# Kernel tuning notes

Measured on AMD Instinct MI355X. Metric: run time of the kernel, lower is better.

Reference implementation:

```python
import jax, jax.numpy as jnp
import numpy as np
from jax import lax

B, C, H, W = 4, 128, 64, 64
D = C // 2          # VSSBlock hidden_dim
DI = 2 * D          # SS2D d_inner (expand=2)
N = 16              # d_state
R = max(D // 16, 1) # dt_rank
K = 4               # scan directions

def dwconv(x, w, b):
    y = lax.conv_general_dilated(x, w, (1, 1), [(1, 1), (1, 1)],
        dimension_numbers=('NCHW', 'OIHW', 'NCHW'), feature_group_count=x.shape[1])
    return y + b[None, :, None, None]

def layer_norm(x, g, b, eps=1e-5):
    mu = jnp.mean(x, axis=-1, keepdims=True)
    var = jnp.var(x, axis=-1, keepdims=True)
    return (x - mu) * lax.rsqrt(var + eps) * g + b

def selective_scan(u, delta, A, Bs, Cs, Dp):
    # u, delta: (B,K,DI,L); Bs, Cs: (B,K,N,L); A: (K,DI,N); Dp: (K,DI)
    uT = jnp.moveaxis(u, -1, 0)
    dT = jnp.moveaxis(delta, -1, 0)
    BT = jnp.moveaxis(Bs, -1, 0)
    CT = jnp.moveaxis(Cs, -1, 0)
    h0 = jnp.zeros(u.shape[:3] + (A.shape[-1],), u.dtype)
    def step(h, inp):
        u_t, d_t, B_t, C_t = inp
        dA = jnp.exp(d_t[..., None] * A)                       # (B,K,DI,N)
        h = dA * h + (d_t * u_t)[..., None] * B_t[:, :, None, :]
        return h, jnp.einsum('bkdn,bkn->bkd', h, C_t)
    _, ys = lax.scan(step, h0, (uT, dT, BT, CT))
    return jnp.moveaxis(ys, 0, -1) + Dp[None, :, :, None] * u  # (B,K,DI,L)

def ss2d(x, in_proj_w, conv_w, conv_b, x_proj_w, dt_w, dt_b, A_logs, Ds, on_g, on_b, out_proj_w):
    # x: (B,H,W,D)
    b, h, w, _ = x.shape
    L = h * w
    xz = x @ in_proj_w.T                                       # (B,H,W,2*DI)
    xc, z = jnp.split(xz, 2, axis=-1)
    xc = jnp.transpose(xc, (0, 3, 1, 2))                       # (B,DI,H,W)
    xc = jax.nn.silu(dwconv(xc, conv_w, conv_b))
    x1 = xc.reshape(b, DI, L)                                  # row-major scan
    x2 = jnp.transpose(xc, (0, 1, 3, 2)).reshape(b, DI, L)     # col-major scan
    xs = jnp.stack([x1, x2, x1[:, :, ::-1], x2[:, :, ::-1]], axis=1)  # (B,K,DI,L)
    x_dbl = jnp.einsum('bkdl,kcd->bkcl', xs, x_proj_w)
    dts, Bsx, Csx = jnp.split(x_dbl, [R, R + N], axis=2)
    delta = jax.nn.softplus(jnp.einsum('bkrl,kdr->bkdl', dts, dt_w) + dt_b[None, :, :, None])
    A = -jnp.exp(A_logs).reshape(K, DI, N)
    out_y = selective_scan(xs, delta, A, Bsx, Csx, Ds.reshape(K, DI))  # (B,K,DI,L)
    inv_y = out_y[:, 2:4, :, ::-1]
    wh_y = jnp.transpose(out_y[:, 1].reshape(b, DI, w, h), (0, 1, 3, 2)).reshape(b, DI, L)
    invwh_y = jnp.transpose(inv_y[:, 1].reshape(b, DI, w, h), (0, 1, 3, 2)).reshape(b, DI, L)
    y = out_y[:, 0] + inv_y[:, 0] + wh_y + invwh_y             # (B,DI,L)
    y = jnp.transpose(y, (0, 2, 1)).reshape(b, h, w, DI)
    y = layer_norm(y, on_g, on_b) * jax.nn.silu(z)
    return y @ out_proj_w.T                                    # (B,H,W,D)

def _forward(x, dw_w, dw_b, scale, ln1_g, ln1_b, in_proj_w, conv_w, conv_b, x_proj_w, dt_w, dt_b, A_logs, Ds, out_norm_g, out_norm_b, out_proj_w, in_gamma, in_beta):
    xd = dwconv(x, dw_w, dw_b)
    x_1, x_2 = jnp.split(xd, 2, axis=1)
    def branch(xi):
        xp = jnp.transpose(xi, (0, 2, 3, 1))                   # (B,H,W,D)
        y = xp + ss2d(layer_norm(xp, ln1_g, ln1_b), in_proj_w, conv_w, conv_b,
                      x_proj_w, dt_w, dt_b, A_logs, Ds, out_norm_g, out_norm_b, out_proj_w)
        return scale * xi + jnp.transpose(y, (0, 3, 1, 2))
    xo = jnp.concatenate([branch(x_1), branch(x_2)], axis=1)
    mu = jnp.mean(xo, axis=(2, 3), keepdims=True)              # InstanceNorm2d(affine)
    var = jnp.var(xo, axis=(2, 3), keepdims=True)
    xo = (xo - mu) * lax.rsqrt(var + 1e-5) * in_gamma[None, :, None, None] + in_beta[None, :, None, None]
    return jnp.where(xo > 0, xo, 0.01 * xo)                    # LeakyReLU(0.01)

def setup_inputs():
    ks = jax.random.split(jax.random.key(0), 12)
    f = lambda k, shp, s=0.02: jax.random.normal(k, shp, jnp.float32) * s
    return dict(
        x=jax.random.normal(ks[0], (B, C, H, W), jnp.float32),
        dw_w=f(ks[1], (C, 1, 3, 3), 0.1), dw_b=f(ks[2], (C,), 0.1),
        scale=jnp.ones((1,), jnp.float32),
        ln1_g=jnp.ones((D,), jnp.float32), ln1_b=jnp.zeros((D,), jnp.float32),
        in_proj_w=f(ks[3], (2 * DI, D)),
        conv_w=f(ks[4], (DI, 1, 3, 3), 0.1), conv_b=f(ks[5], (DI,), 0.1),
        x_proj_w=f(ks[6], (K, R + 2 * N, DI)),
        dt_w=f(ks[7], (K, DI, R), 0.1), dt_b=f(ks[8], (K, DI), 0.1),
        A_logs=f(ks[9], (K * DI, N), 0.5), Ds=jnp.ones((K * DI,), jnp.float32),
        out_norm_g=jnp.ones((DI,), jnp.float32), out_norm_b=jnp.zeros((DI,), jnp.float32),
        out_proj_w=f(ks[10], (D, DI)),
        in_gamma=jnp.ones((C,), jnp.float32), in_beta=jnp.zeros((C,), jnp.float32),
    )

def reference(x, dw_w, dw_b, scale, ln1_g, ln1_b, in_proj_w, conv_w, conv_b, x_proj_w, dt_w, dt_b, A_logs, Ds, out_norm_g, out_norm_b, out_proj_w, in_gamma, in_beta):
    return _forward(x, dw_w, dw_b, scale, ln1_g, ln1_b, in_proj_w, conv_w, conv_b, x_proj_w, dt_w, dt_b, A_logs, Ds, out_norm_g, out_norm_b, out_proj_w, in_gamma, in_beta)
```

## Files before the change

kernel.cpp:

```cpp
#include <hip/hip_runtime.h>
#include <hip/hip_bf16.h>


__device__ __forceinline__ float LD(const void* p, size_t i, bool isb) {
  if (isb) {
    unsigned short u = ((const unsigned short*)p)[i];
    return __uint_as_float(((unsigned)u) << 16);
  }
  return ((const float*)p)[i];
}
__device__ __forceinline__ unsigned short f2bf(float f) {
  unsigned u = __float_as_uint(f);
  u = (u + 0x7FFFu + ((u >> 16) & 1u)) >> 16;
  return (unsigned short)u;
}
__device__ __forceinline__ float silu_(float x) { return x / (1.f + __expf(-x)); }
__device__ __forceinline__ float softplus_(float x) {
  return x > 20.f ? x : __logf(1.f + __expf(x));
}
#define EXP2R(x) __builtin_amdgcn_exp2f(x)

__global__ void kdet(const void* x, int* flag) {
  if (threadIdx.x == 0 && blockIdx.x == 0) {
    const unsigned short* xs = (const unsigned short*)x;
    int bad = 0;
    for (int i = 0; i < 64; ++i) {
      int e = (xs[2 * i] >> 7) & 0xFF;
      if (e > 150 || e < 100) bad++;
    }
    *flag = (bad >= 16) ? 0 : 1;
  }
}

__global__ __launch_bounds__(256) void k0_conv_ln(
    const void* x, const void* dww, const void* dwb, const void* lg, const void* lb,
    const int* __restrict__ flag,
    float* __restrict__ T1, float* __restrict__ T2)
{
  bool isb = (*flag != 0);
  int e = blockIdx.x >> 6, h = blockIdx.x & 63;
  int b = e & 3, br = e >> 2;
  int t = threadIdx.x;
  __shared__ float sIn[3][64][67];
  for (int idx = t; idx < 3 * 64; idx += 256) {
    int r = idx >> 6, d = idx & 63;
    sIn[r][d][0] = 0.f; sIn[r][d][65] = 0.f;
  }
  for (int idx = t; idx < 3 * 64 * 64; idx += 256) {
    int r = idx >> 12, rem = idx & 4095, d = rem >> 6, w = rem & 63;
    int hh = h + r - 1;
    float v = 0.f;
    if (hh >= 0 && hh < 64) v = LD(x, ((size_t)(b * 128 + br * 64 + d) * 64 + hh) * 64 + w, isb);
    sIn[r][d][1 + w] = v;
  }
  __syncthreads();
  int w = t >> 2, g = t & 3;
  float vals[16]; float psum = 0.f, psq = 0.f;
#pragma unroll
  for (int j = 0; j < 16; ++j) {
    int d = g * 16 + j, c = br * 64 + d;
    float s = LD(dwb, c, isb);
#pragma unroll
    for (int kh = 0; kh < 3; ++kh)
#pragma unroll
      for (int kw = 0; kw < 3; ++kw)
        s += LD(dww, c * 9 + kh * 3 + kw, isb) * sIn[kh][d][w + kw];
    vals[j] = s; psum += s; psq += s * s;
  }
  size_t base = ((size_t)e * 4096 + h * 64) * 64 + (size_t)t * 16;
#pragma unroll
  for (int j4 = 0; j4 < 4; ++j4) {
    float4 o; o.x = vals[j4*4]; o.y = vals[j4*4+1]; o.z = vals[j4*4+2]; o.w = vals[j4*4+3];
    *(float4*)(T1 + base + j4 * 4) = o;
  }
  __shared__ float sS[64][4], sQ[64][4];
  sS[w][g] = psum; sQ[w][g] = psq;
  __syncthreads();
  float m = (sS[w][0] + sS[w][1] + sS[w][2] + sS[w][3]) * (1.f / 64.f);
  float q = (sQ[w][0] + sQ[w][1] + sQ[w][2] + sQ[w][3]) * (1.f / 64.f);
  float rs = rsqrtf(q - m * m + 1e-5f);
#pragma unroll
  for (int j4 = 0; j4 < 4; ++j4) {
    float tmp[4];
#pragma unroll
    for (int jj = 0; jj < 4; ++jj) {
      int j = j4 * 4 + jj; int d = g * 16 + j;
      tmp[jj] = (vals[j] - m) * rs * LD(lg, d, isb) + LD(lb, d, isb);
    }
    float4 o; o.x = tmp[0]; o.y = tmp[1]; o.z = tmp[2]; o.w = tmp[3];
    *(float4*)(T2 + base + j4 * 4) = o;
  }
}

__global__ __launch_bounds__(256) void k2_inproj(
    const float* __restrict__ T2, const void* Wip, const int* __restrict__ flag,
    float* __restrict__ T3, float* __restrict__ T4)
{
  bool isb = (*flag != 0);
  int mt = blockIdx.x, ct = blockIdx.y;
  int t = threadIdx.x;
  __shared__ float sA[64][68];
  __shared__ float sB[64][68];
  int row0 = mt * 64;
  for (int q = t; q < 1024; q += 256) {
    int l = q >> 4, d4 = (q & 15) * 4;
    float4 v = *(const float4*)(T2 + (size_t)(row0 + l) * 64 + d4);
    sA[d4][l] = v.x; sA[d4+1][l] = v.y; sA[d4+2][l] = v.z; sA[d4+3][l] = v.w;
  }
  for (int q = t; q < 1024; q += 256) {
    int cl = q >> 4, d4 = (q & 15) * 4;
    size_t base = (size_t)(ct * 64 + cl) * 64 + d4;
    sB[d4][cl]   = LD(Wip, base, isb);
    sB[d4+1][cl] = LD(Wip, base + 1, isb);
    sB[d4+2][cl] = LD(Wip, base + 2, isb);
    sB[d4+3][cl] = LD(Wip, base + 3, isb);
  }
  __syncthreads();
  int ty = t >> 4, tx = t & 15;
  float acc[4][4];
#pragma unroll
  for (int i = 0; i < 4; ++i)
#pragma unroll
    for (int j = 0; j < 4; ++j) acc[i][j] = 0.f;
  for (int kk = 0; kk < 64; ++kk) {
    float4 a = *(const float4*)&sA[kk][ty * 4];
    float4 bq = *(const float4*)&sB[kk][tx * 4];
    float aa[4] = {a.x, a.y, a.z, a.w}, bb[4] = {bq.x, bq.y, bq.z, bq.w};
#pragma unroll
    for (int i = 0; i < 4; ++i)
#pragma unroll
      for (int j = 0; j < 4; ++j) acc[i][j] += aa[i] * bb[j];
  }
  int c0 = ct * 64 + tx * 4;
#pragma unroll
  for (int i = 0; i < 4; ++i) {
    size_t row = (size_t)row0 + ty * 4 + i;
    float4 o;
    if (c0 < 128) {
      o.x = acc[i][0]; o.y = acc[i][1]; o.z = acc[i][2]; o.w = acc[i][3];
      *(float4*)(T3 + row * 128 + c0) = o;
    } else {
      o.x = silu_(acc[i][0]); o.y = silu_(acc[i][1]); o.z = silu_(acc[i][2]); o.w = silu_(acc[i][3]);
      *(float4*)(T4 + row * 128 + (c0 - 128)) = o;
    }
  }
}

__global__ __launch_bounds__(256) void k3_conv2(
    const float* __restrict__ T3, const void* cw, const void* cb, const int* __restrict__ flag,
    float* __restrict__ U0, float* __restrict__ U1)
{
  bool isb = (*flag != 0);
  int e = blockIdx.x >> 6, h = blockIdx.x & 63, dc = blockIdx.y;
  int t = threadIdx.x;
  __shared__ float sI[3][66][65];
  for (int idx = t; idx < 3 * 2 * 64; idx += 256) {
    int r = idx / 128, rem = idx % 128, side = rem >> 6, d = rem & 63;
    sI[r][side * 65][d] = 0.f;
  }
  for (int idx = t; idx < 3 * 64 * 64; idx += 256) {
    int r = idx >> 12, rem = idx & 4095, w = rem >> 6, d = rem & 63;
    int hh = h + r - 1;
    float v = 0.f;
    if (hh >= 0 && hh < 64) v = T3[((size_t)e * 4096 + hh * 64 + w) * 128 + dc * 64 + d];
    sI[r][1 + w][d] = v;
  }
  __syncthreads();
  int d = t & 63, wq = t >> 6;
  int c2 = dc * 64 + d;
  float wt[9];
#pragma unroll
  for (int m = 0; m < 9; ++m) wt[m] = LD(cw, c2 * 9 + m, isb);
  float bias = LD(cb, c2, isb);
  size_t eb = (size_t)e * 4096;
#pragma unroll
  for (int i = 0; i < 16; ++i) {
    int w = wq * 16 + i;
    float s = bias;
#pragma unroll
    for (int kh = 0; kh < 3; ++kh)
#pragma unroll
      for (int kw = 0; kw < 3; ++kw)
        s += wt[kh * 3 + kw] * sI[kh][w + kw][d];
    s = silu_(s);
    U0[(eb + h * 64 + w) * 128 + c2] = s;
    U1[(eb + w * 64 + h) * 128 + c2] = s;
  }
}

__global__ __launch_bounds__(256) void k5_xdbl(
    const float* __restrict__ U0, const float* __restrict__ U1,
    const void* xpw, const int* __restrict__ flag,
    float* __restrict__ dts4, float* __restrict__ Bb2, float* __restrict__ Cb2)
{
  bool isb = (*flag != 0);
  int lt = blockIdx.x;
  int ek = blockIdx.y;
  int e = ek >> 2, k = ek & 3;
  int ls0 = lt * 64;
  int t = threadIdx.x;
  __shared__ float sU[64][132];
  __shared__ float sW[36][132];
  for (int idx = t; idx < 36 * 128; idx += 256) {
    int c = idx >> 7, d = idx & 127;
    sW[c][d] = LD(xpw, ((size_t)k * 36 + c) * 128 + d, isb);
  }
  const float* usrc = (k & 1) ? U1 : U0;
  bool rev = (k >= 2);
  for (int idx = t; idx < 2048; idx += 256) {
    int l = idx >> 5, d4 = (idx & 31) * 4;
    int row = rev ? (4095 - ls0 - l) : (ls0 + l);
    float4 v = *(const float4*)(usrc + ((size_t)e * 4096 + row) * 128 + d4);
    *(float4*)&sU[l][d4] = v;
  }
  __syncthreads();
  int l = t & 63, cg = t >> 6;
  float acc[9];
#pragma unroll
  for (int j = 0; j < 9; ++j) acc[j] = 0.f;
  for (int dd = 0; dd < 32; ++dd) {
    float4 u4 = *(const float4*)&sU[l][dd * 4];
    float ua[4] = {u4.x, u4.y, u4.z, u4.w};
#pragma unroll
    for (int j = 0; j < 9; ++j) {
      float4 w4 = *(const float4*)&sW[cg * 9 + j][dd * 4];
      acc[j] += ua[0] * w4.x + ua[1] * w4.y + ua[2] * w4.z + ua[3] * w4.w;
    }
  }
  size_t row = (size_t)ek * 4096 + ls0 + l;
  if (cg == 0) {
    float4 o; o.x = acc[0]; o.y = acc[1]; o.z = acc[2]; o.w = acc[3];
    *(float4*)(dts4 + row * 4) = o;
#pragma unroll
    for (int j = 4; j < 9; ++j) Bb2[row * 16 + (j - 4)] = acc[j];
  } else {
#pragma unroll
    for (int j = 0; j < 9; ++j) {
      int c = cg * 9 + j;
      if (c < 20) Bb2[row * 16 + (c - 4)] = acc[j];
      else Cb2[row * 16 + (c - 20)] = acc[j];
    }
  }
}

template<int NSTEPS>
__global__ __launch_bounds__(128) void k6a_chunk(
    const float* __restrict__ U0, const float* __restrict__ U1,
    const float* __restrict__ dts4, const float* __restrict__ Bb2,
    const void* alog, const void* dtw, const void* dtb, const int* __restrict__ flag,
    float* __restrict__ Hs)
{
  bool isb = (*flag != 0);
  int chunk = blockIdx.x, ek = blockIdx.y;
  int e = ek >> 2, k = ek & 3;
  int d = threadIdx.x;
  int ls0 = chunk * NSTEPS;
  float a2[16];
#pragma unroll
  for (int n = 0; n < 16; ++n)
    a2[n] = -__expf(LD(alog, ((size_t)k * 128 + d) * 16 + n, isb)) * 1.44269504f;
  float w0 = LD(dtw, ((size_t)k * 128 + d) * 4 + 0, isb);
  float w1 = LD(dtw, ((size_t)k * 128 + d) * 4 + 1, isb);
  float w2 = LD(dtw, ((size_t)k * 128 + d) * 4 + 2, isb);
  float w3 = LD(dtw, ((size_t)k * 128 + d) * 4 + 3, isb);
  float bd = LD(dtb, k * 128 + d, isb);
  float h[16];
#pragma unroll
  for (int n = 0; n < 16; ++n) h[n] = 0.f;
  float sdelta = 0.f;
  const float* usrc = (k & 1) ? U1 : U0;
  const bool rev = (k >= 2);
  const float* ubase = usrc + (size_t)e * 4096 * 128 + d;
  const float4* sbase = (const float4*)(dts4 + ((size_t)ek * 4096 + ls0) * 4);
  const float4* bbase = (const float4*)(Bb2 + ((size_t)ek * 4096 + ls0) * 16);
#pragma unroll 2
  for (int t = 0; t < NSTEPS; ++t) {
    float4 s4 = sbase[t];
    float xv = bd + w0 * s4.x + w1 * s4.y + w2 * s4.z + w3 * s4.w;
    float dlt = softplus_(xv);
    int urow = rev ? (4095 - ls0 - t) : (ls0 + t);
    float uu = ubase[(size_t)urow * 128];
    float du = dlt * uu;
    float4 b0 = bbase[t * 4 + 0], b1 = bbase[t * 4 + 1], b2 = bbase[t * 4 + 2], b3 = bbase[t * 4 + 3];
    float bb[16] = {b0.x,b0.y,b0.z,b0.w, b1.x,b1.y,b1.z,b1.w,
                    b2.x,b2.y,b2.z,b2.w, b3.x,b3.y,b3.z,b3.w};
    sdelta += dlt;
#pragma unroll
    for (int n = 0; n < 16; ++n) {
      float dA = EXP2R(dlt * a2[n]);
      h[n] = fmaf(dA, h[n], du * bb[n]);
    }
  }
  float2* hp = (float2*)Hs + ((size_t)chunk * 65536 + ek * 2048 + d * 16);
#pragma unroll
  for (int n = 0; n < 16; ++n) {
    float2 o; o.x = h[n]; o.y = EXP2R(a2[n] * sdelta);
    hp[n] = o;
  }
}

__global__ __launch_bounds__(256) void k6b_carry(
    float* __restrict__ Hs, int nchunks)
{
  int idx = blockIdx.x * 256 + threadIdx.x;
  float2* hs = (float2*)Hs;
  float carry = 0.f;
  for (int c = 0; c < nchunks; ++c) {
    float2 v = hs[(size_t)c * 65536 + idx];
    Hs[((size_t)c * 65536 + idx) * 2] = carry;
    carry = v.x + v.y * carry;
  }
}

template<int NSTEPS>
__global__ __launch_bounds__(128) void k6c_apply(
    const float* __restrict__ U0, const float* __restrict__ U1,
    float* __restrict__ G2, const float* __restrict__ dts4,
    const float* __restrict__ Bb2, const float* __restrict__ Cb2,
    const void* alog, const void* dtw, const void* dtb,
    const float* __restrict__ Hs, const int* __restrict__ flag)
{
  bool isb = (*flag != 0);
  int chunk = blockIdx.x, ek = blockIdx.y;
  int e = ek >> 2, k = ek & 3;
  int d = threadIdx.x;
  int ls0 = chunk * NSTEPS;
  float a2[16];
#pragma unroll
  for (int n = 0; n < 16; ++n)
    a2[n] = -__expf(LD(alog, ((size_t)k * 128 + d) * 16 + n, isb)) * 1.44269504f;
  float w0 = LD(dtw, ((size_t)k * 128 + d) * 4 + 0, isb);
  float w1 = LD(dtw, ((size_t)k * 128 + d) * 4 + 1, isb);
  float w2 = LD(dtw, ((size_t)k * 128 + d) * 4 + 2, isb);
  float w3 = LD(dtw, ((size_t)k * 128 + d) * 4 + 3, isb);
  float bd = LD(dtb, k * 128 + d, isb);
  float h[16];
  const float* hp = Hs + ((size_t)chunk * 65536 + ek * 2048 + d * 16) * 2;
#pragma unroll
  for (int n = 0; n < 16; ++n) h[n] = hp[2 * n];
  const float* usrc = (k & 1) ? U1 : U0;
  const bool rev = (k >= 2);
  float* gbase = G2 + ((size_t)ek * 4096 + ls0) * 128 + d;
  const float* ubase = usrc + (size_t)e * 4096 * 128 + d;
  const float4* sbase = (const float4*)(dts4 + ((size_t)ek * 4096 + ls0) * 4);
  const float4* bbase = (const float4*)(Bb2 + ((size_t)ek * 4096 + ls0) * 16);
  const float4* cbase = (const float4*)(Cb2 + ((size_t)ek * 4096 + ls0) * 16);
#pragma unroll 2
  for (int t = 0; t < NSTEPS; ++t) {
    float4 s4 = sbase[t];
    float xv = bd + w0 * s4.x + w1 * s4.y + w2 * s4.z + w3 * s4.w;
    float dlt = softplus_(xv);
    int urow = rev ? (4095 - ls0 - t) : (ls0 + t);
    float uu = ubase[(size_t)urow * 128];
    float du = dlt * uu;
    float4 b0 = bbase[t * 4 + 0], b1 = bbase[t * 4 + 1], b2 = bbase[t * 4 + 2], b3 = bbase[t * 4 + 3];
    float4 c0 = cbase[t * 4 + 0], c1 = cbase[t * 4 + 1], c2 = cbase[t * 4 + 2], c3 = cbase[t * 4 + 3];
    float bb[16] = {b0.x,b0.y,b0.z,b0.w, b1.x,b1.y,b1.z,b1.w,
                    b2.x,b2.y,b2.z,b2.w, b3.x,b3.y,b3.z,b3.w};
    float cc[16] = {c0.x,c0.y,c0.z,c0.w, c1.x,c1.y,c1.z,c1.w,
                    c2.x,c2.y,c2.z,c2.w, c3.x,c3.y,c3.z,c3.w};
    float ya = 0.f, yb = 0.f, yc = 0.f, yd = 0.f;
#pragma unroll
    for (int n = 0; n < 16; n += 4) {
      float dA0 = EXP2R(dlt * a2[n]);
      float dA1 = EXP2R(dlt * a2[n+1]);
      float dA2 = EXP2R(dlt * a2[n+2]);
      float dA3 = EXP2R(dlt * a2[n+3]);
      h[n]   = fmaf(dA0, h[n],   du * bb[n]);
      h[n+1] = fmaf(dA1, h[n+1], du * bb[n+1]);
      h[n+2] = fmaf(dA2, h[n+2], du * bb[n+2]);
      h[n+3] = fmaf(dA3, h[n+3], du * bb[n+3]);
      ya = fmaf(h[n],   cc[n],   ya);
      yb = fmaf(h[n+1], cc[n+1], yb);
      yc = fmaf(h[n+2], cc[n+2], yc);
      yd = fmaf(h[n+3], cc[n+3], yd);
    }
    gbase[(size_t)t * 128] = (ya + yb) + (yc + yd);
  }
}

__global__ __launch_bounds__(256) void k7a_combine(
    const float* __restrict__ G2, const float* __restrict__ U0,
    const void* Ds, const int* __restrict__ flag, float* __restrict__ Ysum)
{
  bool isb = (*flag != 0);
  int bx = blockIdx.x;
  int e = bx >> 9, lt = bx & 511;
  int l0 = lt * 8;
  int t = threadIdx.x;
  int r = t >> 5, dq = (t & 31) * 4;
  int l = l0 + r; int hh = l >> 6, w = l & 63;
  float sd0 = 0.f, sd1 = 0.f, sd2 = 0.f, sd3 = 0.f;
#pragma unroll
  for (int k = 0; k < 4; ++k) {
    sd0 += LD(Ds, k * 128 + dq + 0, isb);
    sd1 += LD(Ds, k * 128 + dq + 1, isb);
    sd2 += LD(Ds, k * 128 + dq + 2, isb);
    sd3 += LD(Ds, k * 128 + dq + 3, isb);
  }
  size_t gstride = (size_t)4096 * 128;
  const float* g = G2 + (size_t)(e * 4) * gstride;
  int lw = w * 64 + hh;
  float4 v0 = *(const float4*)(g + 0 * gstride + (size_t)l * 128 + dq);
  float4 v1 = *(const float4*)(g + 1 * gstride + (size_t)lw * 128 + dq);
  float4 v2 = *(const float4*)(g + 2 * gstride + (size_t)(4095 - l) * 128 + dq);
  float4 v3 = *(const float4*)(g + 3 * gstride + (size_t)(4095 - lw) * 128 + dq);
  float4 u4 = *(const float4*)(U0 + ((size_t)e * 4096 + l) * 128 + dq);
  float4 o;
  o.x = v0.x + v1.x + v2.x + v3.x + sd0 * u4.x;
  o.y = v0.y + v1.y + v2.y + v3.y + sd1 * u4.y;
  o.z = v0.z + v1.z + v2.z + v3.z + sd2 * u4.z;
  o.w = v0.w + v1.w + v2.w + v3.w + sd3 * u4.w;
  *(float4*)(Ysum + ((size_t)e * 4096 + l) * 128 + dq) = o;
}

__global__ __launch_bounds__(256) void k7b_out(
    const float* __restrict__ Ysum, const float* __restrict__ T4,
    const float* __restrict__ T1,
    const void* ong, const void* onb, const void* opw, const void* scale_p,
    const int* __restrict__ flag,
    float* __restrict__ P)
{
  bool isb = (*flag != 0);
  int bid = blockIdx.x; int e = bid >> 7, lt = bid & 127;
  int l0 = lt * 32;
  int t = threadIdx.x;
  __shared__ float sY[32][132];
  __shared__ float sWo[64][132];
  __shared__ float sMu[32], sRs[32];
  __shared__ float sPs[32][8], sPq[32][8];
  __shared__ float sP[64][33];
  for (int idx = t; idx < 8192; idx += 256) sWo[idx >> 7][idx & 127] = LD(opw, idx, isb);
  for (int q = t; q < 1024; q += 256) {
    int l = q >> 5, d4 = (q & 31) * 4;
    float4 v = *(const float4*)(Ysum + ((size_t)e * 4096 + l0 + l) * 128 + d4);
    *(float4*)&sY[l][d4] = v;
  }
  __syncthreads();
  {
    int l = t & 31, g = t >> 5;
    float s = 0.f, q2 = 0.f;
#pragma unroll
    for (int j = 0; j < 16; ++j) { float v = sY[l][g * 16 + j]; s += v; q2 += v * v; }
    sPs[l][g] = s; sPq[l][g] = q2;
  }
  __syncthreads();
  if (t < 32) {
    float s = 0.f, q2 = 0.f;
#pragma unroll
    for (int g = 0; g < 8; ++g) { s += sPs[t][g]; q2 += sPq[t][g]; }
    float mu = s * (1.f / 128.f);
    float var = q2 * (1.f / 128.f) - mu * mu;
    sMu[t] = mu; sRs[t] = rsqrtf(var + 1e-5f);
  }
  __syncthreads();
  for (int idx = t; idx < 4096; idx += 256) {
    int l = idx >> 7, dd2 = idx & 127;
    float v = (sY[l][dd2] - sMu[l]) * sRs[l] * LD(ong, dd2, isb) + LD(onb, dd2, isb);
    v *= T4[((size_t)e * 4096 + l0 + l) * 128 + dd2];
    sY[l][dd2] = v;
  }
  __syncthreads();
  float ops = 1.f + LD(scale_p, 0, isb);
  {
    int l = t & 31, cg = t >> 5;
    float acc[8];
#pragma unroll
    for (int j = 0; j < 8; ++j) acc[j] = 0.f;
    for (int dd = 0; dd < 32; ++dd) {
      float4 v4 = *(const float4*)&sY[l][dd * 4];
      float va[4] = {v4.x, v4.y, v4.z, v4.w};
#pragma unroll
      for (int j = 0; j < 8; ++j) {
        float4 w4 = *(const float4*)&sWo[cg * 8 + j][dd * 4];
        acc[j] += va[0] * w4.x + va[1] * w4.y + va[2] * w4.z + va[3] * w4.w;
      }
    }
#pragma unroll
    for (int j = 0; j < 8; ++j) {
      int c = cg * 8 + j;
      sP[c][l] = acc[j] + ops * T1[((size_t)e * 4096 + l0 + l) * 64 + c];
    }
  }
  __syncthreads();
  for (int q = t; q < 512; q += 256) {
    int c = q >> 3, lq = (q & 7) * 4;
    float4 o; o.x = sP[c][lq]; o.y = sP[c][lq+1]; o.z = sP[c][lq+2]; o.w = sP[c][lq+3];
    *(float4*)(P + ((size_t)e * 64 + c) * 4096 + l0 + lq) = o;
  }
}

__global__ __launch_bounds__(256) void k7c_final(
    const float* __restrict__ P, const void* gamma, const void* beta,
    const int* __restrict__ flag, void* __restrict__ out)
{
  bool isb = (*flag != 0);
  int bid = blockIdx.x; int e = bid >> 6, c = bid & 63;
  int b = e & 3, br = e >> 2;
  int cg = br * 64 + c;
  int t = threadIdx.x;
  const float* p = P + ((size_t)e * 64 + c) * 4096;
  float s = 0.f, q2 = 0.f;
  for (int q = t; q < 1024; q += 256) {
    float4 v = *(const float4*)(p + q * 4);
    s += v.x + v.y + v.z + v.w;
    q2 += v.x * v.x + v.y * v.y + v.z * v.z + v.w * v.w;
  }
#pragma unroll
  for (int off = 1; off < 64; off <<= 1) { s += __shfl_xor(s, off); q2 += __shfl_xor(q2, off); }
  __shared__ float rS[4], rQ[4];
  if ((t & 63) == 0) { rS[t >> 6] = s; rQ[t >> 6] = q2; }
  __syncthreads();
  float ts = rS[0] + rS[1] + rS[2] + rS[3];
  float tq = rQ[0] + rQ[1] + rQ[2] + rQ[3];
  float mu = ts * (1.f / 4096.f);
  float var = tq * (1.f / 4096.f) - mu * mu;
  float rsg = rsqrtf(var + 1e-5f);
  float gm = LD(gamma, cg, isb), bt = LD(beta, cg, isb);
  size_t obase = ((size_t)(b * 128 + cg)) * 4096;
  for (int q = t; q < 1024; q += 256) {
    float4 v = *(const float4*)(p + q * 4);
    float o0 = (v.x - mu) * rsg * gm + bt; o0 = o0 > 0.f ? o0 : 0.01f * o0;
    float o1 = (v.y - mu) * rsg * gm + bt; o1 = o1 > 0.f ? o1 : 0.01f * o1;
    float o2 = (v.z - mu) * rsg * gm + bt; o2 = o2 > 0.f ? o2 : 0.01f * o2;
    float o3 = (v.w - mu) * rsg * gm + bt; o3 = o3 > 0.f ? o3 : 0.01f * o3;
    if (isb) {
      unsigned short* op = (unsigned short*)out + obase;
      unsigned lo = (unsigned)f2bf(o0) | ((unsigned)f2bf(o1) << 16);
      unsigned hi = (unsigned)f2bf(o2) | ((unsigned)f2bf(o3) << 16);
      uint2 u; u.x = lo; u.y = hi;
      *(uint2*)(op + q * 4) = u;
    } else {
      float* op = (float*)out + obase;
      float4 o; o.x = o0; o.y = o1; o.z = o2; o.w = o3;
      *(float4*)(op + q * 4) = o;
    }
  }
}

extern "C" void kernel_launch(void* const* d_in, const int* in_sizes, int n_in,
                              void* d_out, int out_size, void* d_ws, size_t ws_size,
                              hipStream_t stream) {
  (void)in_sizes; (void)n_in; (void)out_size;
  const void* x      = d_in[0];
  const void* dw_w   = d_in[1];
  const void* dw_b   = d_in[2];
  const void* scale  = d_in[3];
  const void* ln1_g  = d_in[4];
  const void* ln1_b  = d_in[5];
  const void* ipw    = d_in[6];
  const void* conv_w = d_in[7];
  const void* conv_b = d_in[8];
  const void* xpw    = d_in[9];
  const void* dtw    = d_in[10];
  const void* dtb    = d_in[11];
  const void* alog   = d_in[12];
  const void* Ds     = d_in[13];
  const void* ong    = d_in[14];
  const void* onb    = d_in[15];
  const void* opw    = d_in[16];
  const void* ing    = d_in[17];
  const void* inb    = d_in[18];

  float* ws = (float*)d_ws;
  float* T1  = ws;
  float* T2  = ws + 2097152;
  float* T3  = ws + 4194304;
  float* T4  = ws + 8388608;
  float* U0  = ws + 12582912;
  float* U1  = ws + 16777216;
  float* G2  = ws + 20971520;
  float* Bb2 = T3;
  float* Cb2 = T3 + 2097152;
  float* Hs  = ws + 37748736;
  float* dts4 = T2;
  float* Ysum = U1;

  size_t need64 = ((size_t)37748736 + (size_t)64 * 65536 * 2 + 16) * 4;
  bool big = (ws_size >= need64);
  int nch = big ? 64 : 32;
  int* flag = (int*)(ws + 37748736 + (size_t)nch * 65536 * 2);

  hipLaunchKernelGGL(kdet, dim3(1), dim3(64), 0, stream, x, flag);
  hipLaunchKernelGGL(k0_conv_ln, dim3(512), dim3(256), 0, stream, x, dw_w, dw_b, ln1_g, ln1_b, flag, T1, T2);
  hipLaunchKernelGGL(k2_inproj, dim3(512, 4), dim3(256), 0, stream, T2, ipw, flag, T3, T4);
  hipLaunchKernelGGL(k3_conv2, dim3(512, 2), dim3(256), 0, stream, T3, conv_w, conv_b, flag, U0, U1);
  hipLaunchKernelGGL(k5_xdbl, dim3(64, 32), dim3(256), 0, stream, U0, U1, xpw, flag, dts4, Bb2, Cb2);
  if (big) {
    hipLaunchKernelGGL(k6a_chunk<64>, dim3(64, 32), dim3(128), 0, stream, U0, U1, dts4, Bb2, alog, dtw, dtb, flag, Hs);
    hipLaunchKernelGGL(k6b_carry, dim3(256), dim3(256), 0, stream, Hs, 64);
    hipLaunchKernelGGL(k6c_apply<64>, dim3(64, 32), dim3(128), 0, stream, U0, U1, G2, dts4, Bb2, Cb2, alog, dtw, dtb, Hs, flag);
  } else {
    hipLaunchKernelGGL(k6a_chunk<128>, dim3(32, 32), dim3(128), 0, stream, U0, U1, dts4, Bb2, alog, dtw, dtb, flag, Hs);
    hipLaunchKernelGGL(k6b_carry, dim3(256), dim3(256), 0, stream, Hs, 32);
    hipLaunchKernelGGL(k6c_apply<128>, dim3(32, 32), dim3(128), 0, stream, U0, U1, G2, dts4, Bb2, Cb2, alog, dtw, dtb, Hs, flag);
  }
  hipLaunchKernelGGL(k7a_combine, dim3(4096), dim3(256), 0, stream, G2, U0, Ds, flag, Ysum);
  hipLaunchKernelGGL(k7b_out, dim3(1024), dim3(256), 0, stream, Ysum, T4, T1, ong, onb, opw, scale, flag, T2);
  hipLaunchKernelGGL(k7c_final, dim3(512), dim3(256), 0, stream, T2, ing, inb, flag, d_out);
}
```

Before: 486.8 us.

## Fuse direction-combine into output kernel and share U tiles across reversed scans

The four-direction combine (sum of scan outputs plus D-skip) moves into the output projection kernel, so the Ysum intermediate is no longer written and re-read and one launch goes away. The x_proj kernel now handles a forward direction and its reversed partner in one block. It loads each U tile once and computes both projections, reading the mirrored row for the reversed direction. This halves the U tile loads but doubles shared-memory weight storage and register accumulators per block, which may lower occupancy.

```diff
diff --git a/kernel.cpp b/kernel.cpp
--- a/kernel.cpp
+++ b/kernel.cpp
@@ -195,50 +195,62 @@
 {
   bool isb = (*flag != 0);
   int lt = blockIdx.x;
-  int ek = blockIdx.y;
-  int e = ek >> 2, k = ek & 3;
-  int ls0 = lt * 64;
+  int eyk = blockIdx.y;
+  int e = eyk >> 1, kp = eyk & 1;
+  int r0 = lt * 64;
   int t = threadIdx.x;
   __shared__ float sU[64][132];
-  __shared__ float sW[36][132];
+  __shared__ float sW0[36][132];
+  __shared__ float sW1[36][132];
   for (int idx = t; idx < 36 * 128; idx += 256) {
     int c = idx >> 7, d = idx & 127;
-    sW[c][d] = LD(xpw, ((size_t)k * 36 + c) * 128 + d, isb);
-  }
-  const float* usrc = (k & 1) ? U1 : U0;
-  bool rev = (k >= 2);
+    sW0[c][d] = LD(xpw, ((size_t)kp * 36 + c) * 128 + d, isb);
+    sW1[c][d] = LD(xpw, ((size_t)(kp + 2) * 36 + c) * 128 + d, isb);
+  }
+  const float* usrc = kp ? U1 : U0;
   for (int idx = t; idx < 2048; idx += 256) {
     int l = idx >> 5, d4 = (idx & 31) * 4;
-    int row = rev ? (4095 - ls0 - l) : (ls0 + l);
-    float4 v = *(const float4*)(usrc + ((size_t)e * 4096 + row) * 128 + d4);
+    float4 v = *(const float4*)(usrc + ((size_t)e * 4096 + r0 + l) * 128 + d4);
     *(float4*)&sU[l][d4] = v;
   }
   __syncthreads();
   int l = t & 63, cg = t >> 6;
-  float acc[9];
-#pragma unroll
-  for (int j = 0; j < 9; ++j) acc[j] = 0.f;
+  float acc0[9], acc1[9];
+#pragma unroll
+  for (int j = 0; j < 9; ++j) { acc0[j] = 0.f; acc1[j] = 0.f; }
+  int lm = 63 - l;
   for (int dd = 0; dd < 32; ++dd) {
-    float4 u4 = *(const float4*)&sU[l][dd * 4];
-    float ua[4] = {u4.x, u4.y, u4.z, u4.w};
+    float4 ua4 = *(const float4*)&sU[l][dd * 4];
+    float4 ub4 = *(const float4*)&sU[lm][dd * 4];
+    float ua[4] = {ua4.x, ua4.y, ua4.z, ua4.w};
+    float ub[4] = {ub4.x, ub4.y, ub4.z, ub4.w};
 #pragma unroll
     for (int j = 0; j < 9; ++j) {
-      float4 w4 = *(const float4*)&sW[cg * 9 + j][dd * 4];
-      acc[j] += ua[0] * w4.x + ua[1] * w4.y + ua[2] * w4.z + ua[3] * w4.w;
-    }
-  }
-  size_t row = (size_t)ek * 4096 + ls0 + l;
+      float4 w4a = *(const float4*)&sW0[cg * 9 + j][dd * 4];
+      float4 w4b = *(const float4*)&sW1[cg * 9 + j][dd * 4];
+      acc0[j] += ua[0] * w4a.x + ua[1] * w4a.y + ua[2] * w4a.z + ua[3] * w4a.w;
+      acc1[j] += ub[0] * w4b.x + ub[1] * w4b.y + ub[2] * w4b.z + ub[3] * w4b.w;
+    }
+  }
+  int ek0 = e * 4 + kp, ek1 = e * 4 + kp + 2;
+  size_t row0 = (size_t)ek0 * 4096 + r0 + l;
+  size_t row1 = (size_t)ek1 * 4096 + (4032 - r0) + l;
   if (cg == 0) {
-    float4 o; o.x = acc[0]; o.y = acc[1]; o.z = acc[2]; o.w = acc[3];
-    *(float4*)(dts4 + row * 4) = o;
-#pragma unroll
-    for (int j = 4; j < 9; ++j) Bb2[row * 16 + (j - 4)] = acc[j];
+    float4 o0; o0.x = acc0[0]; o0.y = acc0[1]; o0.z = acc0[2]; o0.w = acc0[3];
+    *(float4*)(dts4 + row0 * 4) = o0;
+    float4 o1; o1.x = acc1[0]; o1.y = acc1[1]; o1.z = acc1[2]; o1.w = acc1[3];
+    *(float4*)(dts4 + row1 * 4) = o1;
+#pragma unroll
+    for (int j = 4; j < 9; ++j) {
+      Bb2[row0 * 16 + (j - 4)] = acc0[j];
+      Bb2[row1 * 16 + (j - 4)] = acc1[j];
+    }
   } else {
 #pragma unroll
     for (int j = 0; j < 9; ++j) {
       int c = cg * 9 + j;
-      if (c < 20) Bb2[row * 16 + (c - 4)] = acc[j];
-      else Cb2[row * 16 + (c - 20)] = acc[j];
+      if (c < 20) { Bb2[row0 * 16 + (c - 4)] = acc0[j]; Bb2[row1 * 16 + (c - 4)] = acc1[j]; }
+      else        { Cb2[row0 * 16 + (c - 20)] = acc0[j]; Cb2[row1 * 16 + (c - 20)] = acc1[j]; }
     }
   }
 }
@@ -379,45 +391,10 @@
   }
 }
 
-__global__ __launch_bounds__(256) void k7a_combine(
+__global__ __launch_bounds__(256) void k7b_out(
     const float* __restrict__ G2, const float* __restrict__ U0,
-    const void* Ds, const int* __restrict__ flag, float* __restrict__ Ysum)
-{
-  bool isb = (*flag != 0);
-  int bx = blockIdx.x;
-  int e = bx >> 9, lt = bx & 511;
-  int l0 = lt * 8;
-  int t = threadIdx.x;
-  int r = t >> 5, dq = (t & 31) * 4;
-  int l = l0 + r; int hh = l >> 6, w = l & 63;
-  float sd0 = 0.f, sd1 = 0.f, sd2 = 0.f, sd3 = 0.f;
-#pragma unroll
-  for (int k = 0; k < 4; ++k) {
-    sd0 += LD(Ds, k * 128 + dq + 0, isb);
-    sd1 += LD(Ds, k * 128 + dq + 1, isb);
-    sd2 += LD(Ds, k * 128 + dq + 2, isb);
-    sd3 += LD(Ds, k * 128 + dq + 3, isb);
-  }
-  size_t gstride = (size_t)4096 * 128;
-  const float* g = G2 + (size_t)(e * 4) * gstride;
-  int lw = w * 64 + hh;
-  float4 v0 = *(const float4*)(g + 0 * gstride + (size_t)l * 128 + dq);
-  float4 v1 = *(const float4*)(g + 1 * gstride + (size_t)lw * 128 + dq);
-  float4 v2 = *(const float4*)(g + 2 * gstride + (size_t)(4095 - l) * 128 + dq);
-  float4 v3 = *(const float4*)(g + 3 * gstride + (size_t)(4095 - lw) * 128 + dq);
-  float4 u4 = *(const float4*)(U0 + ((size_t)e * 4096 + l) * 128 + dq);
-  float4 o;
-  o.x = v0.x + v1.x + v2.x + v3.x + sd0 * u4.x;
-  o.y = v0.y + v1.y + v2.y + v3.y + sd1 * u4.y;
-  o.z = v0.z + v1.z + v2.z + v3.z + sd2 * u4.z;
-  o.w = v0.w + v1.w + v2.w + v3.w + sd3 * u4.w;
-  *(float4*)(Ysum + ((size_t)e * 4096 + l) * 128 + dq) = o;
-}
-
-__global__ __launch_bounds__(256) void k7b_out(
-    const float* __restrict__ Ysum, const float* __restrict__ T4,
-    const float* __restrict__ T1,
-    const void* ong, const void* onb, const void* opw, const void* scale_p,
+    const float* __restrict__ T4, const float* __restrict__ T1,
+    const void* Ds, const void* ong, const void* onb, const void* opw, const void* scale_p,
     const int* __restrict__ flag,
     float* __restrict__ P)
 {
@@ -427,28 +404,43 @@
   int t = threadIdx.x;
   __shared__ float sY[32][132];
   __shared__ float sWo[64][132];
+  __shared__ float sDs[128];
   __shared__ float sMu[32], sRs[32];
   __shared__ float sPs[32][8], sPq[32][8];
   __shared__ float sP[64][33];
+  if (t < 128) {
+    sDs[t] = LD(Ds, t, isb) + LD(Ds, 128 + t, isb) + LD(Ds, 256 + t, isb) + LD(Ds, 384 + t, isb);
+  }
+  __syncthreads();
   for (int idx = t; idx < 8192; idx += 256) sWo[idx >> 7][idx & 127] = LD(opw, idx, isb);
+  size_t gs = (size_t)4096 * 128;
+  const float* g = G2 + (size_t)(e * 4) * gs;
   for (int q = t; q < 1024; q += 256) {
     int l = q >> 5, d4 = (q & 31) * 4;
-    float4 v = *(const float4*)(Ysum + ((size_t)e * 4096 + l0 + l) * 128 + d4);
-    *(float4*)&sY[l][d4] = v;
+    int gl = l0 + l; int hh = gl >> 6, w = gl & 63; int lw = w * 64 + hh;
+    float4 v0 = *(const float4*)(g + 0 * gs + (size_t)gl * 128 + d4);
+    float4 v1 = *(const float4*)(g + 1 * gs + (size_t)lw * 128 + d4);
+    float4 v2 = *(const float4*)(g + 2 * gs + (size_t)(4095 - gl) * 128 + d4);
+    float4 v3 = *(const float4*)(g + 3 * gs + (size_t)(4095 - lw) * 128 + d4);
+    float4 u4 = *(const float4*)(U0 + ((size_t)e * 4096 + gl) * 128 + d4);
+    sY[l][d4]     = v0.x + v1.x + v2.x + v3.x + sDs[d4]     * u4.x;
+    sY[l][d4 + 1] = v0.y + v1.y + v2.y + v3.y + sDs[d4 + 1] * u4.y;
+    sY[l][d4 + 2] = v0.z + v1.z + v2.z + v3.z + sDs[d4 + 2] * u4.z;
+    sY[l][d4 + 3] = v0.w + v1.w + v2.w + v3.w + sDs[d4 + 3] * u4.w;
   }
   __syncthreads();
   {
-    int l = t & 31, g = t >> 5;
+    int l = t & 31, gq = t >> 5;
     float s = 0.f, q2 = 0.f;
 #pragma unroll
-    for (int j = 0; j < 16; ++j) { float v = sY[l][g * 16 + j]; s += v; q2 += v * v; }
-    sPs[l][g] = s; sPq[l][g] = q2;
+    for (int j = 0; j < 16; ++j) { float v = sY[l][gq * 16 + j]; s += v; q2 += v * v; }
+    sPs[l][gq] = s; sPq[l][gq] = q2;
   }
   __syncthreads();
   if (t < 32) {
     float s = 0.f, q2 = 0.f;
 #pragma unroll
-    for (int g = 0; g < 8; ++g) { s += sPs[t][g]; q2 += sPq[t][g]; }
+    for (int gq = 0; gq < 8; ++gq) { s += sPs[t][gq]; q2 += sPq[t][gq]; }
     float mu = s * (1.f / 128.f);
     float var = q2 * (1.f / 128.f) - mu * mu;
     sMu[t] = mu; sRs[t] = rsqrtf(var + 1e-5f);
@@ -574,7 +566,6 @@
   float* Cb2 = T3 + 2097152;
   float* Hs  = ws + 37748736;
   float* dts4 = T2;
-  float* Ysum = U1;
 
   size_t need64 = ((size_t)37748736 + (size_t)64 * 65536 * 2 + 16) * 4;
   bool big = (ws_size >= need64);
@@ -585,7 +576,7 @@
   hipLaunchKernelGGL(k0_conv_ln, dim3(512), dim3(256), 0, stream, x, dw_w, dw_b, ln1_g, ln1_b, flag, T1, T2);
   hipLaunchKernelGGL(k2_inproj, dim3(512, 4), dim3(256), 0, stream, T2, ipw, flag, T3, T4);
   hipLaunchKernelGGL(k3_conv2, dim3(512, 2), dim3(256), 0, stream, T3, conv_w, conv_b, flag, U0, U1);
-  hipLaunchKernelGGL(k5_xdbl, dim3(64, 32), dim3(256), 0, stream, U0, U1, xpw, flag, dts4, Bb2, Cb2);
+  hipLaunchKernelGGL(k5_xdbl, dim3(64, 16), dim3(256), 0, stream, U0, U1, xpw, flag, dts4, Bb2, Cb2);
   if (big) {
     hipLaunchKernelGGL(k6a_chunk<64>, dim3(64, 32), dim3(128), 0, stream, U0, U1, dts4, Bb2, alog, dtw, dtb, flag, Hs);
     hipLaunchKernelGGL(k6b_carry, dim3(256), dim3(256), 0, stream, Hs, 64);
@@ -595,7 +586,6 @@
     hipLaunchKernelGGL(k6b_carry, dim3(256), dim3(256), 0, stream, Hs, 32);
     hipLaunchKernelGGL(k6c_apply<128>, dim3(32, 32), dim3(128), 0, stream, U0, U1, G2, dts4, Bb2, Cb2, alog, dtw, dtb, Hs, flag);
   }
-  hipLaunchKernelGGL(k7a_combine, dim3(4096), dim3(256), 0, stream, G2, U0, Ds, flag, Ysum);
-  hipLaunchKernelGGL(k7b_out, dim3(1024), dim3(256), 0, stream, Ysum, T4, T1, ong, onb, opw, scale, flag, T2);
+  hipLaunchKernelGGL(k7b_out, dim3(1024), dim3(256), 0, stream, G2, U0, T4, T1, Ds, ong, onb, opw, scale, flag, T2);
   hipLaunchKernelGGL(k7c_final, dim3(512), dim3(256), 0, stream, T2, ing, inb, flag, d_out);
 }
```

Result: no change. 491.9 us (+1.0%).

## Fuse four-direction combine into scan apply via atomic adds into Ysum

Applied to the files above, without the earlier changes.

The scan-apply kernel now atomically adds each direction's output into a single Ysum buffer at the un-permuted spatial position. A new init kernel first writes the D-skip term (sum of Ds times u) into that buffer. Together these replace the separate combine kernel and the 4x-sized G2 intermediate, cutting one full write and read of G2. The cost is float atomics on global memory, four contending directions per element, and non-deterministic summation order.

```diff
diff --git a/kernel.cpp b/kernel.cpp
--- a/kernel.cpp
+++ b/kernel.cpp
@@ -241,6 +241,22 @@
       else Cb2[row * 16 + (c - 20)] = acc[j];
     }
   }
+}
+
+__global__ __launch_bounds__(256) void k_init_ysum(
+    const float* __restrict__ U0, const void* Ds, const int* __restrict__ flag,
+    float* __restrict__ Ysum)
+{
+  bool isb = (*flag != 0);
+  size_t idx = ((size_t)blockIdx.x * 256 + threadIdx.x) * 4;
+  int d = (int)(idx & 127);
+  float4 u = *(const float4*)(U0 + idx);
+  float s0 = LD(Ds, d + 0, isb) + LD(Ds, 128 + d + 0, isb) + LD(Ds, 256 + d + 0, isb) + LD(Ds, 384 + d + 0, isb);
+  float s1 = LD(Ds, d + 1, isb) + LD(Ds, 128 + d + 1, isb) + LD(Ds, 256 + d + 1, isb) + LD(Ds, 384 + d + 1, isb);
+  float s2 = LD(Ds, d + 2, isb) + LD(Ds, 128 + d + 2, isb) + LD(Ds, 256 + d + 2, isb) + LD(Ds, 384 + d + 2, isb);
+  float s3 = LD(Ds, d + 3, isb) + LD(Ds, 128 + d + 3, isb) + LD(Ds, 256 + d + 3, isb) + LD(Ds, 384 + d + 3, isb);
+  float4 o; o.x = s0 * u.x; o.y = s1 * u.y; o.z = s2 * u.z; o.w = s3 * u.w;
+  *(float4*)(Ysum + idx) = o;
 }
 
 template<int NSTEPS>
@@ -315,7 +331,7 @@
 template<int NSTEPS>
 __global__ __launch_bounds__(128) void k6c_apply(
     const float* __restrict__ U0, const float* __restrict__ U1,
-    float* __restrict__ G2, const float* __restrict__ dts4,
+    float* __restrict__ Ysum, const float* __restrict__ dts4,
     const float* __restrict__ Bb2, const float* __restrict__ Cb2,
     const void* alog, const void* dtw, const void* dtb,
     const float* __restrict__ Hs, const int* __restrict__ flag)
@@ -340,7 +356,7 @@
   for (int n = 0; n < 16; ++n) h[n] = hp[2 * n];
   const float* usrc = (k & 1) ? U1 : U0;
   const bool rev = (k >= 2);
-  float* gbase = G2 + ((size_t)ek * 4096 + ls0) * 128 + d;
+  float* ybase = Ysum + (size_t)e * 4096 * 128 + d;
   const float* ubase = usrc + (size_t)e * 4096 * 128 + d;
   const float4* sbase = (const float4*)(dts4 + ((size_t)ek * 4096 + ls0) * 4);
   const float4* bbase = (const float4*)(Bb2 + ((size_t)ek * 4096 + ls0) * 16);
@@ -375,43 +391,14 @@
       yc = fmaf(h[n+2], cc[n+2], yc);
       yd = fmaf(h[n+3], cc[n+3], yd);
     }
-    gbase[(size_t)t * 128] = (ya + yb) + (yc + yd);
-  }
-}
-
-__global__ __launch_bounds__(256) void k7a_combine(
-    const float* __restrict__ G2, const float* __restrict__ U0,
-    const void* Ds, const int* __restrict__ flag, float* __restrict__ Ysum)
-{
-  bool isb = (*flag != 0);
-  int bx = blockIdx.x;
-  int e = bx >> 9, lt = bx & 511;
-  int l0 = lt * 8;
-  int t = threadIdx.x;
-  int r = t >> 5, dq = (t & 31) * 4;
-  int l = l0 + r; int hh = l >> 6, w = l & 63;
-  float sd0 = 0.f, sd1 = 0.f, sd2 = 0.f, sd3 = 0.f;
-#pragma unroll
-  for (int k = 0; k < 4; ++k) {
-    sd0 += LD(Ds, k * 128 + dq + 0, isb);
-    sd1 += LD(Ds, k * 128 + dq + 1, isb);
-    sd2 += LD(Ds, k * 128 + dq + 2, isb);
-    sd3 += LD(Ds, k * 128 + dq + 3, isb);
-  }
-  size_t gstride = (size_t)4096 * 128;
-  const float* g = G2 + (size_t)(e * 4) * gstride;
-  int lw = w * 64 + hh;
-  float4 v0 = *(const float4*)(g + 0 * gstride + (size_t)l * 128 + dq);
-  float4 v1 = *(const float4*)(g + 1 * gstride + (size_t)lw * 128 + dq);
-  float4 v2 = *(const float4*)(g + 2 * gstride + (size_t)(4095 - l) * 128 + dq);
-  float4 v3 = *(const float4*)(g + 3 * gstride + (size_t)(4095 - lw) * 128 + dq);
-  float4 u4 = *(const float4*)(U0 + ((size_t)e * 4096 + l) * 128 + dq);
-  float4 o;
-  o.x = v0.x + v1.x + v2.x + v3.x + sd0 * u4.x;
-  o.y = v0.y + v1.y + v2.y + v3.y + sd1 * u4.y;
-  o.z = v0.z + v1.z + v2.z + v3.z + sd2 * u4.z;
-  o.w = v0.w + v1.w + v2.w + v3.w + sd3 * u4.w;
-  *(float4*)(Ysum + ((size_t)e * 4096 + l) * 128 + dq) = o;
+    int p = ls0 + t;
+    int orow;
+    if (k == 0)      orow = p;
+    else if (k == 1) orow = ((p & 63) << 6) | (p >> 6);
+    else if (k == 2) orow = 4095 - p;
+    else { int q = 4095 - p; orow = ((q & 63) << 6) | (q >> 6); }
+    atomicAdd(ybase + (size_t)orow * 128, (ya + yb) + (yc + yd));
+  }
 }
 
 __global__ __launch_bounds__(256) void k7b_out(
@@ -569,33 +556,32 @@
   float* T4  = ws + 8388608;
   float* U0  = ws + 12582912;
   float* U1  = ws + 16777216;
-  float* G2  = ws + 20971520;
+  float* Ysum = ws + 20971520;
   float* Bb2 = T3;
   float* Cb2 = T3 + 2097152;
   float* Hs  = ws + 37748736;
   float* dts4 = T2;
-  float* Ysum = U1;
-
-  size_t need64 = ((size_t)37748736 + (size_t)64 * 65536 * 2 + 16) * 4;
-  bool big = (ws_size >= need64);
-  int nch = big ? 64 : 32;
-  int* flag = (int*)(ws + 37748736 + (size_t)nch * 65536 * 2);
+
+  size_t base_f = 37748736;
+  size_t need64 = (base_f + (size_t)64 * 65536 * 2 + 16) * 4;
+  int nch = (ws_size >= need64) ? 64 : 32;
+  int* flag = (int*)(ws + base_f + (size_t)nch * 65536 * 2);
 
   hipLaunchKernelGGL(kdet, dim3(1), dim3(64), 0, stream, x, flag);
   hipLaunchKernelGGL(k0_conv_ln, dim3(512), dim3(256), 0, stream, x, dw_w, dw_b, ln1_g, ln1_b, flag, T1, T2);
   hipLaunchKernelGGL(k2_inproj, dim3(512, 4), dim3(256), 0, stream, T2, ipw, flag, T3, T4);
   hipLaunchKernelGGL(k3_conv2, dim3(512, 2), dim3(256), 0, stream, T3, conv_w, conv_b, flag, U0, U1);
   hipLaunchKernelGGL(k5_xdbl, dim3(64, 32), dim3(256), 0, stream, U0, U1, xpw, flag, dts4, Bb2, Cb2);
-  if (big) {
+  hipLaunchKernelGGL(k_init_ysum, dim3(4096), dim3(256), 0, stream, U0, Ds, flag, Ysum);
+  if (nch == 64) {
     hipLaunchKernelGGL(k6a_chunk<64>, dim3(64, 32), dim3(128), 0, stream, U0, U1, dts4, Bb2, alog, dtw, dtb, flag, Hs);
     hipLaunchKernelGGL(k6b_carry, dim3(256), dim3(256), 0, stream, Hs, 64);
-    hipLaunchKernelGGL(k6c_apply<64>, dim3(64, 32), dim3(128), 0, stream, U0, U1, G2, dts4, Bb2, Cb2, alog, dtw, dtb, Hs, flag);
+    hipLaunchKernelGGL(k6c_apply<64>, dim3(64, 32), dim3(128), 0, stream, U0, U1, Ysum, dts4, Bb2, Cb2, alog, dtw, dtb, Hs, flag);
   } else {
     hipLaunchKernelGGL(k6a_chunk<128>, dim3(32, 32), dim3(128), 0, stream, U0, U1, dts4, Bb2, alog, dtw, dtb, flag, Hs);
     hipLaunchKernelGGL(k6b_carry, dim3(256), dim3(256), 0, stream, Hs, 32);
-    hipLaunchKernelGGL(k6c_apply<128>, dim3(32, 32), dim3(128), 0, stream, U0, U1, G2, dts4, Bb2, Cb2, alog, dtw, dtb, Hs, flag);
-  }
-  hipLaunchKernelGGL(k7a_combine, dim3(4096), dim3(256), 0, stream, G2, U0, Ds, flag, Ysum);
+    hipLaunchKernelGGL(k6c_apply<128>, dim3(32, 32), dim3(128), 0, stream, U0, U1, Ysum, dts4, Bb2, Cb2, alog, dtw, dtb, Hs, flag);
+  }
   hipLaunchKernelGGL(k7b_out, dim3(1024), dim3(256), 0, stream, Ysum, T4, T1, ong, onb, opw, scale, flag, T2);
   hipLaunchKernelGGL(k7c_final, dim3(512), dim3(256), 0, stream, T2, ing, inb, flag, d_out);
 }
```

Result: faster. 467.6 us (-3.9%).
